# Kernel tuning notes

Hardware: AMD Instinct MI355X
Metric: run time of the kernel (lower is better)

The kernel has to match this reference:

```python
import jax, jax.numpy as jnp
import numpy as np

B, S, D, H, F = 2, 2048, 1024, 16, 4096
DK = D // H
EPS = 1e-6


def _ln(x, g, b):
    mu = jnp.mean(x, axis=-1, keepdims=True)
    var = jnp.mean(jnp.square(x - mu), axis=-1, keepdims=True)
    return (x - mu) * jax.lax.rsqrt(var + EPS) * g + b


def setup_inputs() -> dict:
    key = jax.random.key(0)
    ks = jax.random.split(key, 8)
    sc = 0.02
    return {
        "x": jax.random.normal(ks[0], (B, S, D), jnp.float32),
        "wq": jax.random.normal(ks[1], (D, D), jnp.float32) * sc,
        "bq": jnp.zeros((D,), jnp.float32),
        "wk": jax.random.normal(ks[2], (D, D), jnp.float32) * sc,
        "bk": jnp.zeros((D,), jnp.float32),
        "wv": jax.random.normal(ks[3], (D, D), jnp.float32) * sc,
        "bv": jnp.zeros((D,), jnp.float32),
        "wo": jax.random.normal(ks[4], (D, D), jnp.float32) * sc,
        "bo": jnp.zeros((D,), jnp.float32),
        "w1": jax.random.normal(ks[5], (D, F), jnp.float32) * sc,
        "b1": jnp.zeros((F,), jnp.float32),
        "w2": jax.random.normal(ks[6], (F, D), jnp.float32) * sc,
        "b2": jnp.zeros((D,), jnp.float32),
        "g1": jnp.ones((D,), jnp.float32),
        "be1": jnp.zeros((D,), jnp.float32),
        "g2": jnp.ones((D,), jnp.float32),
        "be2": jnp.zeros((D,), jnp.float32),
    }


def reference(x, wq, bq, wk, bk, wv, bv, wo, bo, w1, b1, w2, b2, g1, be1, g2, be2):
    # Multi-head self-attention (no masks, eval-mode dropout = identity)
    q = (x @ wq + bq).reshape(B, S, H, DK)
    k = (x @ wk + bk).reshape(B, S, H, DK)
    v = (x @ wv + bv).reshape(B, S, H, DK)
    scale = 1.0 / (DK ** 0.5)
    score = jnp.einsum('bihd,bjhd->bhij', q, k) * scale  # [B,H,S,S]
    p = jax.nn.softmax(score, axis=-1)
    attn = jnp.einsum('bhij,bjhd->bihd', p, v).reshape(B, S, D)
    attn = attn @ wo + bo
    # residual + LayerNorm 1
    h = _ln(x + attn, g1, be1)
    # FFN (relu) + residual + LayerNorm 2
    ff = jax.nn.relu(h @ w1 + b1) @ w2 + b2
    return _ln(h + ff, g2, be2)
```

## Files before the change

### kernel.cpp

```cpp
#include <hip/hip_runtime.h>
#include <hip/hip_bf16.h>
#include <cmath>

typedef __bf16 bf16_t;
typedef __bf16 bf16x4 __attribute__((ext_vector_type(4)));
typedef __bf16 bf16x8 __attribute__((ext_vector_type(8)));
typedef float  f32x4  __attribute__((ext_vector_type(4)));

__device__ __forceinline__ void gld_lds16(const bf16_t* g, bf16_t* l) {
    __builtin_amdgcn_global_load_lds(
        (const __attribute__((address_space(1))) void*)g,
        (__attribute__((address_space(3))) void*)l,
        16, 0, 0);
}


struct PrepArgs {
    const float* w[6]; bf16_t* wt[6];
    int K[6], N[6], start[6];
    const float* x; bf16_t* xb; int castStart;
    const float* bq; const float* bk; float* bqkv; int biasStart;
};

__global__ __launch_bounds__(256) void prep(PrepArgs pa) {
    __shared__ float tile[32][33];
    const int bid = blockIdx.x, t = threadIdx.x;
    if (bid < pa.castStart) {
        int mi = 0;
#pragma unroll
        for (int i = 1; i < 6; i++) if (bid >= pa.start[i]) mi = i;
        const int tt  = bid - pa.start[mi];
        const int nbx = pa.N[mi] >> 5;
        const int n0 = (tt % nbx) * 32, k0 = (tt / nbx) * 32;
        const float* in = pa.w[mi];
        bf16_t* out = pa.wt[mi];
        const int K = pa.K[mi], N = pa.N[mi];
        const int tx = t & 31, ty = t >> 5;
#pragma unroll
        for (int i = 0; i < 4; i++) {
            int kk = ty + i * 8;
            tile[kk][tx] = in[(size_t)(k0 + kk) * N + n0 + tx];
        }
        __syncthreads();
#pragma unroll
        for (int i = 0; i < 4; i++) {
            int nn = ty + i * 8;
            out[(size_t)(n0 + nn) * K + k0 + tx] = (bf16_t)tile[tx][nn];
        }
    } else if (bid < pa.biasStart) {
        int i = (bid - pa.castStart) * 256 + t;
        f32x4 v = ((const f32x4*)pa.x)[i];
        bf16x4 o;
        o[0] = (bf16_t)v[0]; o[1] = (bf16_t)v[1]; o[2] = (bf16_t)v[2]; o[3] = (bf16_t)v[3];
        ((bf16x4*)pa.xb)[i] = o;
    } else {
#pragma unroll
        for (int j = 0; j < 8; j++) {
            int idx = t * 8 + j;
            pa.bqkv[idx] = idx < 1024 ? pa.bq[idx] : pa.bk[idx - 1024];
        }
    }
}

template<int BN>
__global__ __launch_bounds__(512, 1) void gemm_deep(
    const bf16_t* __restrict__ A, const bf16_t* __restrict__ Bt,
    const float* __restrict__ bias,
    float* __restrict__ Cf, bf16_t* __restrict__ Cb,
    int M, int N, int lda, int Kloc, int relu, int nbn) {
    constexpr int NT = BN / 64;
    constexpr int WN = BN / 4;
    __shared__ __attribute__((aligned(16))) bf16_t As[4][256 * 32];
    __shared__ __attribute__((aligned(16))) bf16_t Bs[4][BN * 32];
    const int tid  = threadIdx.x;
    const int lane = tid & 63;
    const int wave = tid >> 6;
    const int wm = wave >> 2, wn = wave & 3;
    const int kh = blockIdx.z;

    const int span  = 8 * nbn;
    const int group = blockIdx.x / span;
    const int rem   = blockIdx.x % span;
    const int bm    = group * 8 + (rem & 7);
    const int bn    = rem >> 3;

    float*  Cf_b = Cf ? Cf + (size_t)kh * M * N : nullptr;
    const int koff = kh * Kloc;

    const int srow   = tid >> 2;
    const int slot_s = ((tid & 3) ^ ((tid >> 3) & 3)) * 8;
    const bf16_t* Ag = A  + (size_t)(bm * 256 + srow) * lda + koff + slot_s;
    const bf16_t* Bg = Bt + (size_t)(bn * BN  + srow) * lda + koff + slot_s;

    auto stage = [&](int kk, int buf) {
        gld_lds16(Ag + kk,                       &As[buf][0]        + tid * 8);
        gld_lds16(Ag + (size_t)128 * lda + kk,   &As[buf][128 * 32] + tid * 8);
        gld_lds16(Bg + kk,                       &Bs[buf][0]        + tid * 8);
        if constexpr (BN == 256)
            gld_lds16(Bg + (size_t)128 * lda + kk, &Bs[buf][128 * 32] + tid * 8);
    };

    f32x4 acc[8][NT] = {};
    const int mrow = lane & 15;
    const int qsw  = (((lane >> 4) ^ ((mrow >> 1) & 3))) * 8;

    auto compute = [&](int cur) {
        bf16x8 bfr[NT], af[8];
#pragma unroll
        for (int n = 0; n < NT; n++)
            bfr[n] = *(const bf16x8*)(&Bs[cur][(wn * WN + n * 16 + mrow) * 32 + qsw]);
#pragma unroll
        for (int mt = 0; mt < 8; mt++)
            af[mt] = *(const bf16x8*)(&As[cur][(wm * 128 + mt * 16 + mrow) * 32 + qsw]);
        __builtin_amdgcn_s_setprio(1);
#pragma unroll
        for (int mt = 0; mt < 8; mt++)
#pragma unroll
            for (int n = 0; n < NT; n++)
                acc[mt][n] = __builtin_amdgcn_mfma_f32_16x16x32_bf16(
                    af[mt], bfr[n], acc[mt][n], 0, 0, 0);
        __builtin_amdgcn_s_setprio(0);
    };

    stage(0, 0); stage(32, 1); stage(64, 2);
    const int nst = Kloc >> 5;
    for (int t = 0; t + 3 < nst; ++t) {
        stage((t + 3) * 32, (t + 3) & 3);
        if constexpr (BN == 256) asm volatile("s_waitcnt vmcnt(12)" ::: "memory");
        else                     asm volatile("s_waitcnt vmcnt(9)"  ::: "memory");
        __builtin_amdgcn_s_barrier();
        compute(t & 3);
        asm volatile("s_waitcnt lgkmcnt(0)" ::: "memory");
        __builtin_amdgcn_s_barrier();
    }
    if constexpr (BN == 256) asm volatile("s_waitcnt vmcnt(8)" ::: "memory");
    else                     asm volatile("s_waitcnt vmcnt(6)" ::: "memory");
    __builtin_amdgcn_s_barrier();
    compute((nst - 3) & 3);
    asm volatile("s_waitcnt lgkmcnt(0)" ::: "memory");
    __builtin_amdgcn_s_barrier();
    if constexpr (BN == 256) asm volatile("s_waitcnt vmcnt(4)" ::: "memory");
    else                     asm volatile("s_waitcnt vmcnt(3)" ::: "memory");
    __builtin_amdgcn_s_barrier();
    compute((nst - 2) & 3);
    asm volatile("s_waitcnt lgkmcnt(0)" ::: "memory");
    __builtin_amdgcn_s_barrier();
    asm volatile("s_waitcnt vmcnt(0)" ::: "memory");
    __builtin_amdgcn_s_barrier();
    compute((nst - 1) & 3);

    const int rq = (lane >> 4) * 4;
#pragma unroll
    for (int mt = 0; mt < 8; mt++) {
        int row0 = bm * 256 + wm * 128 + mt * 16 + rq;
#pragma unroll
        for (int n = 0; n < NT; n++) {
            int col = bn * BN + wn * WN + n * 16 + mrow;
            float bvc = (bias && kh == 0) ? bias[col] : 0.f;
#pragma unroll
            for (int r = 0; r < 4; r++) {
                float v = acc[mt][n][r] + bvc;
                if (relu) v = fmaxf(v, 0.f);
                size_t idx = (size_t)(row0 + r) * N + col;
                if (Cf_b) Cf_b[idx] = v;
                if (Cb)   Cb[idx]   = (bf16_t)v;
            }
        }
    }
}

template<int BN>
__global__ __launch_bounds__(512, 2) void gemm_bt256(
    const bf16_t* __restrict__ A, const bf16_t* __restrict__ Bt,
    const float* __restrict__ bias,
    float* __restrict__ Cf, bf16_t* __restrict__ Cb,
    int M, int N, int lda, int Kloc, int relu, int nbn,
    long bt_bstride, long c_bstride) {
    constexpr int NT = BN / 64;
    constexpr int WN = BN / 4;
    __shared__ __attribute__((aligned(16))) bf16_t As[2][2][256 * 32];
    __shared__ __attribute__((aligned(16))) bf16_t Bs[2][2][BN * 32];
    const int tid  = threadIdx.x;
    const int lane = tid & 63;
    const int wave = tid >> 6;
    const int wm = wave >> 2, wn = wave & 3;
    const int kh = blockIdx.z;

    const int span  = 8 * nbn;
    const int group = blockIdx.x / span;
    const int rem   = blockIdx.x % span;
    const int bm    = group * 8 + (rem & 7);
    const int bn    = rem >> 3;

    const bf16_t* Bt_b = Bt + (size_t)blockIdx.y * bt_bstride;
    float*  Cf_b = Cf ? Cf + (size_t)blockIdx.y * c_bstride + (size_t)kh * M * N : nullptr;
    bf16_t* Cb_b = Cb ? Cb + (size_t)blockIdx.y * c_bstride : nullptr;
    const int koff = kh * Kloc;

    const int r4 = tid >> 2;
    const int kcs = ((tid & 3) ^ ((tid >> 3) & 3)) * 8;
    const bf16_t* Ag = A    + (size_t)(bm * 256 + r4) * lda + koff + kcs;
    const bf16_t* Bg = Bt_b + (size_t)(bn * BN  + r4) * lda + koff + kcs;

    f32x4 acc[8][NT] = {};
    const int mrow = lane & 15;
    const int qsw  = (((lane >> 4) ^ ((mrow >> 1) & 3))) * 8;

    auto stage = [&](int kk, int buf) {
#pragma unroll
        for (int hh = 0; hh < 2; hh++) {
#pragma unroll
            for (int i = 0; i < 2; i++)
                gld_lds16(Ag + (size_t)(i * 128) * lda + kk + hh * 32,
                          &As[buf][hh][i * 128 * 32] + tid * 8);
            if (BN == 256) {
#pragma unroll
                for (int i = 0; i < 2; i++)
                    gld_lds16(Bg + (size_t)(i * 128) * lda + kk + hh * 32,
                              &Bs[buf][hh][i * 128 * 32] + tid * 8);
            } else {
                gld_lds16(Bg + kk + hh * 32, &Bs[buf][hh][0] + tid * 8);
            }
        }
    };

    stage(0, 0);
    __syncthreads();

    const int nsteps = Kloc >> 6;
    for (int st = 0; st < nsteps; ++st) {
        const int cur = st & 1;
        if (st + 1 < nsteps) stage((st + 1) << 6, cur ^ 1);

#pragma unroll
        for (int hh = 0; hh < 2; hh++) {
            bf16x8 bfr[NT];
#pragma unroll
            for (int n = 0; n < NT; n++)
                bfr[n] = *(const bf16x8*)(&Bs[cur][hh][(wn * WN + n * 16 + mrow) * 32 + qsw]);
#pragma unroll
            for (int mt = 0; mt < 8; mt++) {
                bf16x8 af = *(const bf16x8*)(&As[cur][hh][(wm * 128 + mt * 16 + mrow) * 32 + qsw]);
#pragma unroll
                for (int n = 0; n < NT; n++)
                    acc[mt][n] = __builtin_amdgcn_mfma_f32_16x16x32_bf16(
                        af, bfr[n], acc[mt][n], 0, 0, 0);
            }
        }
        __syncthreads();
    }

    const int rq = (lane >> 4) * 4;
#pragma unroll
    for (int mt = 0; mt < 8; mt++) {
        int row0 = bm * 256 + wm * 128 + mt * 16 + rq;
#pragma unroll
        for (int n = 0; n < NT; n++) {
            int col = bn * BN + wn * WN + n * 16 + mrow;
            float bvc = (bias && kh == 0) ? bias[col] : 0.f;
#pragma unroll
            for (int r = 0; r < 4; r++) {
                float v = acc[mt][n][r] + bvc;
                if (relu) v = fmaxf(v, 0.f);
                size_t idx = (size_t)(row0 + r) * N + col;
                if (Cf_b) Cf_b[idx] = v;
                if (Cb_b) Cb_b[idx] = (bf16_t)v;
            }
        }
    }
}

template<int MT>
__global__ __launch_bounds__(256) void gemm_bt(
    const bf16_t* __restrict__ A, const bf16_t* __restrict__ Bt,
    const float* __restrict__ bias,
    float* __restrict__ Cf, bf16_t* __restrict__ Cb,
    int M, int N, int lda, int Kloc, int relu, int nbn, int bias_row,
    long bt_bstride, long c_bstride) {
    constexpr int TM = MT * 32;
    __shared__ __attribute__((aligned(16))) bf16_t As[2][TM * 32];
    __shared__ __attribute__((aligned(16))) bf16_t Bs[2][128 * 32];
    const int tid  = threadIdx.x;
    const int lane = tid & 63;
    const int wave = tid >> 6;
    const int wm = wave & 1, wn = wave >> 1;
    const int kh = blockIdx.z;

    const int span  = 8 * nbn;
    const int group = blockIdx.x / span;
    const int rem   = blockIdx.x % span;
    const int bm    = group * 8 + (rem & 7);
    const int bn    = rem >> 3;

    const bf16_t* Bt_b = Bt + (size_t)blockIdx.y * bt_bstride;
    float*  Cf_b = Cf ? Cf + (size_t)blockIdx.y * c_bstride + (size_t)kh * M * N : nullptr;
    bf16_t* Cb_b = Cb ? Cb + (size_t)blockIdx.y * c_bstride : nullptr;
    const int koff = kh * Kloc;

    const int r4 = tid >> 2;
    const int kcs = ((tid & 3) ^ ((tid >> 3) & 3)) * 8;
    const bf16_t* Ag = A    + (size_t)(bm * TM  + r4) * lda + koff + kcs;
    const bf16_t* Bg = Bt_b + (size_t)(bn * 128 + r4) * lda + koff + kcs;

    f32x4 acc[MT][4] = {};
    const int mrow = lane & 15;
    const int qsw  = (((lane >> 4) ^ ((mrow >> 1) & 3))) * 8;

    auto stage = [&](int kk, int buf) {
#pragma unroll
        for (int i = 0; i < MT / 2; i++)
            gld_lds16(Ag + (size_t)(i * 64) * lda + kk, &As[buf][i * 64 * 32] + tid * 8);
        gld_lds16(Bg + kk,                        &Bs[buf][0] + tid * 8);
        gld_lds16(Bg + (size_t)64 * lda + kk,     &Bs[buf][64 * 32] + tid * 8);
    };

    stage(0, 0);
    __syncthreads();

    const int nt = Kloc >> 5;
    for (int t7 = 0; t7 < nt; ++t7) {
        const int cur = t7 & 1;
        if (t7 + 1 < nt) stage((t7 + 1) << 5, cur ^ 1);

        bf16x8 af[MT], bfr[4];
#pragma unroll
        for (int mt = 0; mt < MT; mt++)
            af[mt] = *(const bf16x8*)(&As[cur][(wm * (MT * 16) + mt * 16 + mrow) * 32 + qsw]);
#pragma unroll
        for (int nt2 = 0; nt2 < 4; nt2++)
            bfr[nt2] = *(const bf16x8*)(&Bs[cur][(wn * 64 + nt2 * 16 + mrow) * 32 + qsw]);
#pragma unroll
        for (int mt = 0; mt < MT; mt++)
#pragma unroll
            for (int nt2 = 0; nt2 < 4; nt2++)
                acc[mt][nt2] = __builtin_amdgcn_mfma_f32_16x16x32_bf16(
                    af[mt], bfr[nt2], acc[mt][nt2], 0, 0, 0);

        __syncthreads();
    }

    const int rq = (lane >> 4) * 4;
#pragma unroll
    for (int mt = 0; mt < MT; mt++) {
        int row0 = bm * TM + wm * (MT * 16) + mt * 16 + rq;
#pragma unroll
        for (int nt2 = 0; nt2 < 4; nt2++) {
            int col = bn * 128 + wn * 64 + nt2 * 16 + mrow;
            float bvc = (bias && kh == 0 && !bias_row) ? bias[col] : 0.f;
#pragma unroll
            for (int r = 0; r < 4; r++) {
                float bb = (bias && kh == 0 && bias_row) ? bias[row0 + r] : bvc;
                float v = acc[mt][nt2][r] + bb;
                if (relu) v = fmaxf(v, 0.f);
                size_t idx = (size_t)(row0 + r) * N + col;
                if (Cf_b) Cf_b[idx] = v;
                if (Cb_b) Cb_b[idx] = (bf16_t)v;
            }
        }
    }
}

__global__ __launch_bounds__(512) void flash_attn_mfma(
    const bf16_t* __restrict__ QKb,
    const bf16_t* __restrict__ Vtg,
    bf16_t* __restrict__ Outb) {
    __shared__ __attribute__((aligned(16))) bf16_t Ks[2][4096];
    __shared__ __attribute__((aligned(16))) bf16_t Vs[2][4096];
    __shared__ __attribute__((aligned(16))) bf16_t Ps[8192];
    const int t = threadIdx.x;
    const int lane = t & 63, wave = t >> 6;
    const int g = lane >> 4, cl = lane & 15;
    const int b = blockIdx.z, h = blockIdx.y, q0 = blockIdx.x * 128;
    const int RS = 2048;
    const bf16_t* Qg = QKb + (size_t)(b * 2048 + q0) * RS + h * 64;
    const bf16_t* Kg = QKb + (size_t)(b * 2048) * RS + 1024 + h * 64;
    const bf16_t* Vg = Vtg + ((size_t)b * 1024 + h * 64) * 2048;

    const int sr   = (t >> 2) & 63;
    const int half = t >> 8;
    const int scs  = half * 32 + (((t & 3) ^ ((t >> 3) & 3)) * 8);

    const float C = 0.125f * 1.4426950408889634f;
    const bf16_t* Qrow = Qg + (size_t)(wave * 16 + cl) * RS;
    bf16x8 qr0 = *(const bf16x8*)(Qrow + g * 8);
    bf16x8 qr1 = *(const bf16x8*)(Qrow + 32 + g * 8);
#pragma unroll
    for (int j = 0; j < 8; j++) {
        qr0[j] = (bf16_t)((float)qr0[j] * C);
        qr1[j] = (bf16_t)((float)qr1[j] * C);
    }

    const bf16_t* Kst = Kg + (size_t)sr * RS + scs;
    const bf16_t* Vst = Vg + (size_t)sr * 2048 + scs;

    gld_lds16(Kst, &Ks[0][0] + t * 8);
    gld_lds16(Vst, &Vs[0][0] + t * 8);
    __syncthreads();

    f32x4 Oacc[4] = {};
    f32x4 Lacc = {};
    bf16x8 ones;
#pragma unroll
    for (int j = 0; j < 8; j++) ones[j] = (bf16_t)1.0f;

    const int rowb = wave * 16 + cl;
    const int psw  = (cl & 7) << 4;
    const int gsw  = ((g ^ ((cl >> 1) & 3))) * 8;
    char* PsB = (char*)Ps;

    for (int kt_i = 0; kt_i < 32; ++kt_i) {
        const int cur = kt_i & 1;
        if (kt_i + 1 < 32) {
            Kst += (size_t)64 * RS;
            Vst += 64;
            gld_lds16(Kst, &Ks[cur ^ 1][0] + t * 8);
            gld_lds16(Vst, &Vs[cur ^ 1][0] + t * 8);
        }

        f32x4 Sacc[4] = {};
        __builtin_amdgcn_s_setprio(1);
#pragma unroll
        for (int ks = 0; ks < 2; ++ks) {
            bf16x8 bq = ks ? qr1 : qr0;
#pragma unroll
            for (int mt = 0; mt < 4; ++mt) {
                bf16x8 ak = *(const bf16x8*)(&Ks[cur][ks * 2048 + (mt * 16 + cl) * 32 + gsw]);
                Sacc[mt] = __builtin_amdgcn_mfma_f32_16x16x32_bf16(ak, bq, Sacc[mt], 0, 0, 0);
            }
        }
        __builtin_amdgcn_s_setprio(0);

#pragma unroll
        for (int mt = 0; mt < 4; ++mt) {
            bf16x4 p4;
#pragma unroll
            for (int r = 0; r < 4; r++)
                p4[r] = (bf16_t)__builtin_amdgcn_exp2f(Sacc[mt][r]);
            *(bf16x4*)(PsB + ((rowb * 128 + mt * 32 + g * 8) ^ psw)) = p4;
        }

        __builtin_amdgcn_s_setprio(1);
#pragma unroll
        for (int ks = 0; ks < 2; ++ks) {
            bf16x8 ap = *(const bf16x8*)(PsB + ((rowb * 128 + ks * 64 + g * 16) ^ psw));
            Lacc = __builtin_amdgcn_mfma_f32_16x16x32_bf16(ap, ones, Lacc, 0, 0, 0);
#pragma unroll
            for (int nt = 0; nt < 4; ++nt) {
                bf16x8 bv = *(const bf16x8*)(&Vs[cur][ks * 2048 + (nt * 16 + cl) * 32 + gsw]);
                Oacc[nt] = __builtin_amdgcn_mfma_f32_16x16x32_bf16(ap, bv, Oacc[nt], 0, 0, 0);
            }
        }
        __builtin_amdgcn_s_setprio(0);

        __syncthreads();
    }

#pragma unroll
    for (int r = 0; r < 4; r++) {
        float inv = 1.f / Lacc[r];
        int qrow = q0 + wave * 16 + g * 4 + r;
        size_t base = (size_t)(b * 2048 + qrow) * 1024 + h * 64;
#pragma unroll
        for (int nt = 0; nt < 4; nt++)
            Outb[base + nt * 16 + cl] = (bf16_t)(Oacc[nt][r] * inv);
    }
}

__global__ __launch_bounds__(256) void resid_ln3(const float* __restrict__ a,
                                                 const float* __restrict__ p0,
                                                 const float* __restrict__ p1,
                                                 const float* __restrict__ g,
                                                 const float* __restrict__ be,
                                                 float* __restrict__ outf,
                                                 bf16_t* __restrict__ outb) {
    const int row = blockIdx.x, t = threadIdx.x;
    const size_t base = (size_t)row * 1024;
    f32x4 v = ((const f32x4*)(a + base))[t] + ((const f32x4*)(p0 + base))[t];
    if (p1) v += ((const f32x4*)(p1 + base))[t];
    float sum = v[0] + v[1] + v[2] + v[3];
    float sq  = v[0] * v[0] + v[1] * v[1] + v[2] * v[2] + v[3] * v[3];
#pragma unroll
    for (int o = 1; o < 64; o <<= 1) {
        sum += __shfl_xor(sum, o);
        sq  += __shfl_xor(sq, o);
    }
    __shared__ float red[8];
    int wave = t >> 6, lane = t & 63;
    if (lane == 0) { red[wave] = sum; red[4 + wave] = sq; }
    __syncthreads();
    sum = red[0] + red[1] + red[2] + red[3];
    sq  = red[4] + red[5] + red[6] + red[7];
    float mu  = sum * (1.f / 1024.f);
    float var = sq * (1.f / 1024.f) - mu * mu;
    float rs  = rsqrtf(var + 1e-6f);
    f32x4 g4 = ((const f32x4*)g)[t];
    f32x4 b4 = ((const f32x4*)be)[t];
    f32x4 o = (v - mu) * rs * g4 + b4;
    ((f32x4*)(outf + base))[t] = o;
    if (outb) {
        bf16x4 ob;
        ob[0] = (bf16_t)o[0]; ob[1] = (bf16_t)o[1]; ob[2] = (bf16_t)o[2]; ob[3] = (bf16_t)o[3];
        ((bf16x4*)(outb + base))[t] = ob;
    }
}

extern "C" void kernel_launch(void* const* d_in, const int* in_sizes, int n_in,
                              void* d_out, int out_size, void* d_ws, size_t ws_size,
                              hipStream_t stream) {
    (void)in_sizes; (void)n_in; (void)out_size; (void)ws_size;
    const float* x   = (const float*)d_in[0];
    const float* wq  = (const float*)d_in[1];
    const float* bq  = (const float*)d_in[2];
    const float* wk  = (const float*)d_in[3];
    const float* bk  = (const float*)d_in[4];
    const float* wv  = (const float*)d_in[5];
    const float* bv  = (const float*)d_in[6];
    const float* wo  = (const float*)d_in[7];
    const float* bo  = (const float*)d_in[8];
    const float* w1  = (const float*)d_in[9];
    const float* b1  = (const float*)d_in[10];
    const float* w2  = (const float*)d_in[11];
    const float* b2  = (const float*)d_in[12];
    const float* g1  = (const float*)d_in[13];
    const float* be1 = (const float*)d_in[14];
    const float* g2  = (const float*)d_in[15];
    const float* be2 = (const float*)d_in[16];
    float* out = (float*)d_out;

    char* ws = (char*)d_ws;
    const size_t MB = 1ull << 20;
    bf16_t* xb    = (bf16_t*)(ws + 0);
    bf16_t* WtQKV = (bf16_t*)(ws + 8 * MB);
    bf16_t* WtO   = (bf16_t*)(ws + 14 * MB);
    bf16_t* Wt1   = (bf16_t*)(ws + 16 * MB);
    bf16_t* Wt2   = (bf16_t*)(ws + 24 * MB);
    float*  bqkv  = (float*)(ws + 32 * MB);
    bf16_t* QKb   = (bf16_t*)(ws + 33 * MB);
    bf16_t* Vt    = (bf16_t*)(ws + 49 * MB);
    bf16_t* ffb   = (bf16_t*)(ws + 33 * MB);
    float*  oa    = (float*)(ws + 65 * MB);
    float*  f2    = (float*)(ws + 65 * MB);
    float*  hbuf  = (float*)(ws + 97 * MB);
    bf16_t* hb    = (bf16_t*)(ws + 113 * MB);
    bf16_t* ab    = xb;
    const int MN = 4096 * 1024;

    PrepArgs pa;
    pa.w[0] = wq; pa.w[1] = wk; pa.w[2] = wv; pa.w[3] = wo; pa.w[4] = w1; pa.w[5] = w2;
    pa.wt[0] = WtQKV; pa.wt[1] = WtQKV + 1024 * 1024; pa.wt[2] = WtQKV + 2048 * 1024;
    pa.wt[3] = WtO; pa.wt[4] = Wt1; pa.wt[5] = Wt2;
    int Ks[6] = {1024, 1024, 1024, 1024, 1024, 4096};
    int Ns[6] = {1024, 1024, 1024, 1024, 4096, 1024};
    int st[6] = {0, 1024, 2048, 3072, 4096, 8192};
    for (int i = 0; i < 6; i++) { pa.K[i] = Ks[i]; pa.N[i] = Ns[i]; pa.start[i] = st[i]; }
    pa.x = x; pa.xb = xb; pa.castStart = 12288;
    pa.bq = bq; pa.bk = bk; pa.bqkv = bqkv; pa.biasStart = 12288 + 4096;
    prep<<<12288 + 4096 + 1, 256, 0, stream>>>(pa);

    gemm_bt256<128><<<256, 512, 0, stream>>>(xb, WtQKV, bqkv, nullptr, QKb,
                                        4096, 2048, 1024, 1024, 0, 16, 0, 0);
    gemm_bt<2><<<dim3(256, 2, 1), 256, 0, stream>>>(WtQKV + 2048 * 1024, xb, bv,
                                        nullptr, Vt, 1024, 2048, 1024, 1024, 0, 16, 1,
                                        (long)2048 * 1024, (long)1024 * 2048);
    flash_attn_mfma<<<dim3(16, 16, 2), 512, 0, stream>>>(QKb, Vt, ab);
    gemm_bt256<128><<<dim3(128, 1, 2), 512, 0, stream>>>(ab, WtO, bo, oa, nullptr,
                                        4096, 1024, 1024, 512, 0, 8, 0, 0);
    resid_ln3<<<4096, 256, 0, stream>>>(x, oa, oa + MN, g1, be1, hbuf, hb);
    gemm_deep<256><<<256, 512, 0, stream>>>(hb, Wt1, b1, nullptr, ffb,
                                        4096, 4096, 1024, 1024, 1, 16);
    gemm_bt256<128><<<dim3(128, 1, 2), 512, 0, stream>>>(ffb, Wt2, b2, f2, nullptr,
                                        4096, 1024, 4096, 2048, 0, 8, 0, 0);
    resid_ln3<<<4096, 256, 0, stream>>>(hbuf, f2, f2 + MN, g2, be2, out, nullptr);
}
```

Measured before the change: 381.9 us.

## Triple-buffer gemm_bt256 with explicit vmcnt waits and MFMA priority boost

Turns the BN=128 GEMM's double-buffered LDS pipeline into a three-stage pipeline that keeps two tiles of global-to-LDS loads in flight. It synchronises with explicit s_waitcnt vmcnt/lgkmcnt plus raw s_barrier in place of __syncthreads. It also raises wave priority around the MFMA block and drops the unused template and batch-stride parameters. LDS use grows to 144KB, so launch bounds fall to one block per CU, trading occupancy for deeper prefetch. The hand-tuned vmcnt counts depend on exactly six loads per stage.

Measured after the change: 381.7 us. Within noise of the previous version (-0.1%).

```diff
diff --git a/kernel.cpp b/kernel.cpp
--- a/kernel.cpp
+++ b/kernel.cpp
@@ -169,17 +169,14 @@
     }
 }
 
-template<int BN>
-__global__ __launch_bounds__(512, 2) void gemm_bt256(
+__global__ __launch_bounds__(512, 1) void gemm_bt256(
     const bf16_t* __restrict__ A, const bf16_t* __restrict__ Bt,
     const float* __restrict__ bias,
     float* __restrict__ Cf, bf16_t* __restrict__ Cb,
-    int M, int N, int lda, int Kloc, int relu, int nbn,
-    long bt_bstride, long c_bstride) {
-    constexpr int NT = BN / 64;
-    constexpr int WN = BN / 4;
-    __shared__ __attribute__((aligned(16))) bf16_t As[2][2][256 * 32];
-    __shared__ __attribute__((aligned(16))) bf16_t Bs[2][2][BN * 32];
+    int M, int N, int lda, int Kloc, int relu, int nbn) {
+    constexpr int BN = 128, NT = 2, WN = 32;
+    __shared__ __attribute__((aligned(16))) bf16_t As[3][2][256 * 32];
+    __shared__ __attribute__((aligned(16))) bf16_t Bs[3][2][BN * 32];
     const int tid  = threadIdx.x;
     const int lane = tid & 63;
     const int wave = tid >> 6;
@@ -192,15 +189,13 @@
     const int bm    = group * 8 + (rem & 7);
     const int bn    = rem >> 3;
 
-    const bf16_t* Bt_b = Bt + (size_t)blockIdx.y * bt_bstride;
-    float*  Cf_b = Cf ? Cf + (size_t)blockIdx.y * c_bstride + (size_t)kh * M * N : nullptr;
-    bf16_t* Cb_b = Cb ? Cb + (size_t)blockIdx.y * c_bstride : nullptr;
+    float*  Cf_b = Cf ? Cf + (size_t)kh * M * N : nullptr;
     const int koff = kh * Kloc;
 
     const int r4 = tid >> 2;
     const int kcs = ((tid & 3) ^ ((tid >> 3) & 3)) * 8;
-    const bf16_t* Ag = A    + (size_t)(bm * 256 + r4) * lda + koff + kcs;
-    const bf16_t* Bg = Bt_b + (size_t)(bn * BN  + r4) * lda + koff + kcs;
+    const bf16_t* Ag = A  + (size_t)(bm * 256 + r4) * lda + koff + kcs;
+    const bf16_t* Bg = Bt + (size_t)(bn * BN  + r4) * lda + koff + kcs;
 
     f32x4 acc[8][NT] = {};
     const int mrow = lane & 15;
@@ -213,31 +208,18 @@
             for (int i = 0; i < 2; i++)
                 gld_lds16(Ag + (size_t)(i * 128) * lda + kk + hh * 32,
                           &As[buf][hh][i * 128 * 32] + tid * 8);
-            if (BN == 256) {
-#pragma unroll
-                for (int i = 0; i < 2; i++)
-                    gld_lds16(Bg + (size_t)(i * 128) * lda + kk + hh * 32,
-                              &Bs[buf][hh][i * 128 * 32] + tid * 8);
-            } else {
-                gld_lds16(Bg + kk + hh * 32, &Bs[buf][hh][0] + tid * 8);
-            }
+            gld_lds16(Bg + kk + hh * 32, &Bs[buf][hh][0] + tid * 8);
         }
     };
 
-    stage(0, 0);
-    __syncthreads();
-
-    const int nsteps = Kloc >> 6;
-    for (int st = 0; st < nsteps; ++st) {
-        const int cur = st & 1;
-        if (st + 1 < nsteps) stage((st + 1) << 6, cur ^ 1);
-
+    auto compute = [&](int cur) {
 #pragma unroll
         for (int hh = 0; hh < 2; hh++) {
             bf16x8 bfr[NT];
 #pragma unroll
             for (int n = 0; n < NT; n++)
                 bfr[n] = *(const bf16x8*)(&Bs[cur][hh][(wn * WN + n * 16 + mrow) * 32 + qsw]);
+            __builtin_amdgcn_s_setprio(1);
 #pragma unroll
             for (int mt = 0; mt < 8; mt++) {
                 bf16x8 af = *(const bf16x8*)(&As[cur][hh][(wm * 128 + mt * 16 + mrow) * 32 + qsw]);
@@ -246,9 +228,29 @@
                     acc[mt][n] = __builtin_amdgcn_mfma_f32_16x16x32_bf16(
                         af, bfr[n], acc[mt][n], 0, 0, 0);
             }
-        }
-        __syncthreads();
-    }
+            __builtin_amdgcn_s_setprio(0);
+        }
+    };
+
+    stage(0, 0); stage(64, 1);
+    const int nst = Kloc >> 6;
+    int t = 0;
+    for (; t + 2 < nst; ++t) {
+        stage((t + 2) << 6, (t + 2) % 3);
+        asm volatile("s_waitcnt vmcnt(12)" ::: "memory");
+        __builtin_amdgcn_s_barrier();
+        compute(t % 3);
+        asm volatile("s_waitcnt lgkmcnt(0)" ::: "memory");
+        __builtin_amdgcn_s_barrier();
+    }
+    asm volatile("s_waitcnt vmcnt(6)" ::: "memory");
+    __builtin_amdgcn_s_barrier();
+    compute((nst - 2) % 3);
+    asm volatile("s_waitcnt lgkmcnt(0)" ::: "memory");
+    __builtin_amdgcn_s_barrier();
+    asm volatile("s_waitcnt vmcnt(0)" ::: "memory");
+    __builtin_amdgcn_s_barrier();
+    compute((nst - 1) % 3);
 
     const int rq = (lane >> 4) * 4;
 #pragma unroll
@@ -264,7 +266,7 @@
                 if (relu) v = fmaxf(v, 0.f);
                 size_t idx = (size_t)(row0 + r) * N + col;
                 if (Cf_b) Cf_b[idx] = v;
-                if (Cb_b) Cb_b[idx] = (bf16_t)v;
+                if (Cb)   Cb[idx]   = (bf16_t)v;
             }
         }
     }
@@ -557,18 +559,18 @@
     pa.bq = bq; pa.bk = bk; pa.bqkv = bqkv; pa.biasStart = 12288 + 4096;
     prep<<<12288 + 4096 + 1, 256, 0, stream>>>(pa);
 
-    gemm_bt256<128><<<256, 512, 0, stream>>>(xb, WtQKV, bqkv, nullptr, QKb,
-                                        4096, 2048, 1024, 1024, 0, 16, 0, 0);
+    gemm_bt256<<<256, 512, 0, stream>>>(xb, WtQKV, bqkv, nullptr, QKb,
+                                        4096, 2048, 1024, 1024, 0, 16);
     gemm_bt<2><<<dim3(256, 2, 1), 256, 0, stream>>>(WtQKV + 2048 * 1024, xb, bv,
                                         nullptr, Vt, 1024, 2048, 1024, 1024, 0, 16, 1,
                                         (long)2048 * 1024, (long)1024 * 2048);
     flash_attn_mfma<<<dim3(16, 16, 2), 512, 0, stream>>>(QKb, Vt, ab);
-    gemm_bt256<128><<<dim3(128, 1, 2), 512, 0, stream>>>(ab, WtO, bo, oa, nullptr,
-                                        4096, 1024, 1024, 512, 0, 8, 0, 0);
+    gemm_bt256<<<dim3(128, 1, 2), 512, 0, stream>>>(ab, WtO, bo, oa, nullptr,
+                                        4096, 1024, 1024, 512, 0, 8);
     resid_ln3<<<4096, 256, 0, stream>>>(x, oa, oa + MN, g1, be1, hbuf, hb);
     gemm_deep<256><<<256, 512, 0, stream>>>(hb, Wt1, b1, nullptr, ffb,
                                         4096, 4096, 1024, 1024, 1, 16);
-    gemm_bt256<128><<<dim3(128, 1, 2), 512, 0, stream>>>(ffb, Wt2, b2, f2, nullptr,
-                                        4096, 1024, 4096, 2048, 0, 8, 0, 0);
+    gemm_bt256<<<dim3(128, 1, 2), 512, 0, stream>>>(ffb, Wt2, b2, f2, nullptr,
+                                        4096, 1024, 4096, 2048, 0, 8);
     resid_ln3<<<4096, 256, 0, stream>>>(hbuf, f2, f2 + MN, g2, be2, out, nullptr);
 }
```
